# Kernel tuning notes

Hardware: AMD Instinct MI355X
Metric: run time of the kernel (lower is better)

The kernel has to match this reference:

```python
import jax, jax.numpy as jnp
import numpy as np

N = 50000   # nodes
E = 200000  # triplets
IN = 128    # num_in_features
H = 4       # heads
F = 64      # num_out_features
HID = 64    # attention_mlp_hidden


def setup_inputs() -> dict:
    key = jax.random.key(0)
    ks = jax.random.split(key, 12)
    rn = lambda k, shape, s=0.05: (jax.random.normal(k, shape, jnp.float32) * s)
    return {
        "in_nodes_features": jax.random.normal(ks[0], (N, IN), jnp.float32),
        "edge_index": jax.random.randint(ks[1], (3, E), 0, N, jnp.int32),
        "W_proj": rn(ks[2], (H * F, IN)),          # linear_proj (no bias)
        "att_W1": rn(ks[3], (HID, 3 * F)),
        "att_b1": jnp.zeros((HID,), jnp.float32),
        "att_W2": rn(ks[4], (1, HID)),
        "att_b2": jnp.zeros((1,), jnp.float32),
        "e_W1": rn(ks[5], (F, 2 * F)),
        "e_b1": jnp.zeros((F,), jnp.float32),
        "e_W2": rn(ks[6], (F, F)),
        "e_b2": jnp.zeros((F,), jnp.float32),
        "theta": rn(ks[7], (1, H, F), 0.1),
        "bias": jnp.zeros((H * F,), jnp.float32),
    }


def _edge_nn(pair, e_W1, e_b1, e_W2, e_b2):
    # pair: [E, H, 2F] -> [E, H, F]
    h = jax.nn.leaky_relu(jnp.einsum('ehc,fc->ehf', pair, e_W1) + e_b1, 0.2)
    return jnp.einsum('ehf,gf->ehg', h, e_W2) + e_b2


def reference(in_nodes_features, edge_index, W_proj, att_W1, att_b1, att_W2,
              att_b2, e_W1, e_b1, e_W2, e_b2, theta, bias):
    proj = (in_nodes_features @ W_proj.T).reshape(-1, H, F)  # [N, H, F]
    pi = proj[edge_index[0]]  # [E, H, F]
    pj = proj[edge_index[1]]
    pk = proj[edge_index[2]]

    # attention MLP on concatenated triplet features
    comb = jnp.concatenate([pi, pj, pk], axis=-1)            # [E, H, 3F]
    h = jax.nn.relu(jnp.einsum('ehc,dc->ehd', comb, att_W1) + att_b1)
    scores = (jnp.einsum('ehd,od->eho', h, att_W2) + att_b2)[..., 0]  # [E, H]
    scores = jax.nn.leaky_relu(scores, 0.2)
    att = jax.nn.softmax(scores, axis=-1)[..., None]         # softmax over heads, [E, H, 1]

    pairs = [(pj, pk), (pi, pk), (pi, pj)]
    outs = []
    for i in range(3):
        prod = _edge_nn(jnp.concatenate(pairs[i], axis=-1), e_W1, e_b1, e_W2, e_b2)
        ws = jax.ops.segment_sum(att * prod, edge_index[i], num_segments=proj.shape[0])
        outs.append(theta * proj + ws)                       # [N, H, F]

    out = jnp.concatenate(outs, axis=0).reshape(-1, H * F)   # [3N, H*F]
    out = out + bias
    return jax.nn.elu(out)
```

## Files before the change

kernel.cpp:

```cpp
#include <hip/hip_runtime.h>
#include <hip/hip_bf16.h>

#define N_NODES 50000
#define N_EDGES 200000
#define IN_F 128
#define HEADS 4
#define FD 64
#define HF 256
#define NCOLS 1536
#define NT3 (3 * N_NODES)
#define E3  (3 * N_EDGES)
#define TROW 320

#define OFF_PROJ   0UL
#define OFF_TABS   51200000UL
#define OFF_ATT    179200000UL
#define OFF_RANK   182400000UL
#define OFF_ELIST  184800000UL
#define OFF_CNT    187200000UL
#define OFF_OFFS   187800000UL
#define OFF_BSUM   188400008UL
#define OFF_BSW    188401040UL
#define OFF_CB     188794256UL

typedef __attribute__((ext_vector_type(8))) short short8;
typedef __attribute__((ext_vector_type(4))) float f32x4;

__device__ inline short bf16_of(float x) {
    __hip_bfloat16 h = __float2bfloat16(x);
    return *reinterpret_cast<short*>(&h);
}
__device__ inline unsigned pack2(float lo, float hi) {
    return ((unsigned)(unsigned short)bf16_of(hi) << 16) |
           (unsigned)(unsigned short)bf16_of(lo);
}
__device__ inline short8 pack8(float4 a, float4 b) {
    short8 o;
    o[0] = bf16_of(a.x); o[1] = bf16_of(a.y); o[2] = bf16_of(a.z); o[3] = bf16_of(a.w);
    o[4] = bf16_of(b.x); o[5] = bf16_of(b.y); o[6] = bf16_of(b.z); o[7] = bf16_of(b.w);
    return o;
}
__device__ inline void unpk(uint4 v, float* f) {
    f[0] = __uint_as_float(v.x << 16); f[1] = __uint_as_float(v.x & 0xffff0000u);
    f[2] = __uint_as_float(v.y << 16); f[3] = __uint_as_float(v.y & 0xffff0000u);
    f[4] = __uint_as_float(v.z << 16); f[5] = __uint_as_float(v.z & 0xffff0000u);
    f[6] = __uint_as_float(v.w << 16); f[7] = __uint_as_float(v.w & 0xffff0000u);
}
__device__ inline float score8(uint4 ua, uint4 ub, uint4 uc, const float* w) {
    float fa[8], fb[8], fc[8]; unpk(ua, fa); unpk(ub, fb); unpk(uc, fc);
    float p = 0.f;
#pragma unroll
    for (int j = 0; j < 8; ++j) {
        float x = fa[j] + fb[j] + fc[j];
        x = fmaxf(x, 0.f);
        p = fmaf(x, w[j], p);
    }
    return p;
}

__global__ __launch_bounds__(128) void k_comp(const float* __restrict__ Wp,
                                              const float* __restrict__ attW1,
                                              const float* __restrict__ eW1,
                                              const float* __restrict__ attb1,
                                              const float* __restrict__ eb1,
                                              __hip_bfloat16* __restrict__ Bsw,
                                              float* __restrict__ colbias) {
    const int c = blockIdx.x;
    const int k = threadIdx.x;
    float acc;
    float cb = 0.f;
    if (c < HF) {
        acc = Wp[c * IN_F + k];
    } else {
        const int t = (c - HF) >> 8;
        const int rem = (c - HF) & 255;
        const int h = rem >> 6, g = rem & 63;
        const float* T;
        if (t == 0)      T = attW1 + g * 192;
        else if (t == 1) T = attW1 + g * 192 + 64;
        else if (t == 2) T = attW1 + g * 192 + 128;
        else if (t == 3) T = eW1 + g * 128;
        else             T = eW1 + g * 128 + 64;
        acc = 0.f;
        for (int f = 0; f < 64; ++f)
            acc += T[f] * Wp[(h * 64 + f) * IN_F + k];
        if (t == 0) cb = attb1[g];
        else if (t == 3) cb = eb1[g];
    }
    const int ct = c >> 4, cin = c & 15, kin = k & 31, j = k & 7;
    const int ks = k >> 5;
    const int l = cin + ((kin >> 3) << 4);
    Bsw[((ct * 4 + ks) * 64 + l) * 8 + j] = __float2bfloat16(acc);
    if (k == 0) colbias[c] = cb;
}

__global__ __launch_bounds__(256) void k_tab(const float* __restrict__ in,
                                             const __hip_bfloat16* __restrict__ BswH,
                                             const float* __restrict__ colbias,
                                             float* __restrict__ proj,
                                             __hip_bfloat16* __restrict__ tabs) {
    const short8* Bsw = reinterpret_cast<const short8*>(BswH);
    const int lane = threadIdx.x & 63;
    const int wv = threadIdx.x >> 6;
    const int r = lane & 15, q = lane >> 4;
    const int row0 = blockIdx.x * 16;

    short8 a[4];
    const float* ip = in + (size_t)(row0 + r) * IN_F + q * 8;
#pragma unroll
    for (int ks = 0; ks < 4; ++ks)
        a[ks] = pack8(*(const float4*)(ip + ks * 32), *(const float4*)(ip + ks * 32 + 4));

    for (int ctl = 0; ctl < 24; ++ctl) {
        const int ct = wv * 24 + ctl;
        const int c = ct * 16 + r;
        const float cb = colbias[c];
        f32x4 acc = {cb, cb, cb, cb};
#pragma unroll
        for (int ks = 0; ks < 4; ++ks)
            acc = __builtin_amdgcn_mfma_f32_16x16x32_bf16(a[ks], Bsw[(ct * 4 + ks) * 64 + lane], acc, 0, 0, 0);
        if (c < HF) {
#pragma unroll
            for (int i = 0; i < 4; ++i)
                proj[(size_t)(row0 + q * 4 + i) * HF + c] = acc[i];
        } else {
            const int t = (c - HF) >> 8;
            const int rem = (c - HF) & 255;
            const int h = rem >> 6, g = rem & 63;
#pragma unroll
            for (int i = 0; i < 4; ++i)
                tabs[(((size_t)(row0 + q * 4 + i) * HEADS + h) * 5 + t) * 64 + g] =
                    __float2bfloat16(acc[i]);
        }
    }
}

__global__ __launch_bounds__(256) void k_hist(const int* __restrict__ eidx,
                                              int* __restrict__ cnt,
                                              int* __restrict__ rank) {
    const int g = blockIdx.x * 256 + threadIdx.x;
    if (g < E3) {
        const int node = eidx[g];
        const int t = g / N_EDGES;
        rank[g] = atomicAdd(&cnt[t * N_NODES + node], 1);
    }
}

__global__ __launch_bounds__(256) void k_scan1(const int* __restrict__ cnt,
                                               int* __restrict__ offs,
                                               int* __restrict__ bsums) {
    __shared__ int lds[256];
    const int b = blockIdx.x, t = threadIdx.x;
    const int base = b * 1024 + t * 4;
    int v[4];
#pragma unroll
    for (int c = 0; c < 4; ++c) v[c] = (base + c < NT3) ? cnt[base + c] : 0;
    const int s = v[0] + v[1] + v[2] + v[3];
    lds[t] = s;
    __syncthreads();
    for (int off = 1; off < 256; off <<= 1) {
        int x = (t >= off) ? lds[t - off] : 0;
        __syncthreads();
        lds[t] += x;
        __syncthreads();
    }
    if (t == 255) bsums[b] = lds[255];
    int run = lds[t] - s;
#pragma unroll
    for (int c = 0; c < 4; ++c) {
        if (base + c < NT3) offs[base + c] = run;
        run += v[c];
    }
}

__global__ __launch_bounds__(256) void k_scan2(int* __restrict__ bsums, int nb) {
    __shared__ int lds[256];
    const int t = threadIdx.x;
    const int v = (t < nb) ? bsums[t] : 0;
    lds[t] = v;
    __syncthreads();
    for (int off = 1; off < 256; off <<= 1) {
        int x = (t >= off) ? lds[t - off] : 0;
        __syncthreads();
        lds[t] += x;
        __syncthreads();
    }
    if (t < nb) bsums[t] = lds[t] - v;
}

__global__ __launch_bounds__(256) void k_scan3(int* __restrict__ offs,
                                               const int* __restrict__ bsums) {
    const int i = blockIdx.x * 256 + threadIdx.x;
    if (i < NT3) offs[i] += bsums[i >> 10];
    if (i == NT3) offs[NT3] = E3;
}

__global__ __launch_bounds__(256) void k_scat(const int* __restrict__ eidx,
                                              const int* __restrict__ offs,
                                              const int* __restrict__ rank,
                                              int* __restrict__ elist) {
    const int g = blockIdx.x * 256 + threadIdx.x;
    if (g < E3) {
        const int node = eidx[g];
        const int t = g / N_EDGES;
        const int e = g - t * N_EDGES;
        elist[offs[t * N_NODES + node] + rank[g]] = e;
    }
}

__global__ __launch_bounds__(256) void k_att(
        const int* __restrict__ eidx,
        const __hip_bfloat16* __restrict__ tabs,
        const float* __restrict__ attW2, const float* __restrict__ attb2,
        float* __restrict__ attbuf) {
    __shared__ float s_lds[HEADS][16];
    const int lane = threadIdx.x & 63;
    const int h = threadIdx.x >> 6;
    const int r = lane & 15, q = lane >> 4;
    const int e0 = blockIdx.x * 16;

    float awlo[8], awhi[8];
    {
        float4 w0 = *(const float4*)(attW2 + q * 8);
        float4 w1 = *(const float4*)(attW2 + q * 8 + 4);
        awlo[0] = w0.x; awlo[1] = w0.y; awlo[2] = w0.z; awlo[3] = w0.w;
        awlo[4] = w1.x; awlo[5] = w1.y; awlo[6] = w1.z; awlo[7] = w1.w;
        float4 w2 = *(const float4*)(attW2 + 32 + q * 8);
        float4 w3 = *(const float4*)(attW2 + 32 + q * 8 + 4);
        awhi[0] = w2.x; awhi[1] = w2.y; awhi[2] = w2.z; awhi[3] = w2.w;
        awhi[4] = w3.x; awhi[5] = w3.y; awhi[6] = w3.z; awhi[7] = w3.w;
    }
    const float ab2s = attb2[0];

    const int ni = eidx[e0 + r];
    const int nj = eidx[N_EDGES + e0 + r];
    const int nk = eidx[2 * N_EDGES + e0 + r];

    const size_t bi = ((size_t)ni * HEADS + h) * TROW + q * 8;
    const size_t bj = ((size_t)nj * HEADS + h) * TROW + q * 8;
    const size_t bk = ((size_t)nk * HEADS + h) * TROW + q * 8;

    uint4 a0 = *(const uint4*)(tabs + bi);
    uint4 a1 = *(const uint4*)(tabs + bi + 32);
    uint4 b0 = *(const uint4*)(tabs + bj + 64);
    uint4 b1 = *(const uint4*)(tabs + bj + 96);
    uint4 c0 = *(const uint4*)(tabs + bk + 128);
    uint4 c1 = *(const uint4*)(tabs + bk + 160);

    float p = score8(a0, b0, c0, awlo) + score8(a1, b1, c1, awhi);
    p += __shfl_xor(p, 16);
    p += __shfl_xor(p, 32);
    float sc = p + ab2s;
    sc = fmaxf(sc, 0.2f * sc);
    if (lane < 16) s_lds[h][lane] = sc;
    __syncthreads();
    if (lane < 16) {
        const float s0 = s_lds[0][lane], s1 = s_lds[1][lane];
        const float s2 = s_lds[2][lane], s3 = s_lds[3][lane];
        const float mx = fmaxf(fmaxf(s0, s1), fmaxf(s2, s3));
        const float x0 = __expf(s0 - mx), x1 = __expf(s1 - mx);
        const float x2 = __expf(s2 - mx), x3 = __expf(s3 - mx);
        const float rs = 1.f / (x0 + x1 + x2 + x3);
        const float xh = (h == 0) ? x0 : (h == 1) ? x1 : (h == 2) ? x2 : x3;
        attbuf[(size_t)(e0 + lane) * 4 + h] = xh * rs;
    }
}

__global__ __launch_bounds__(256) void k_seg(const int* __restrict__ eidx,
                                             const int* __restrict__ offs,
                                             const int* __restrict__ elist,
                                             const float* __restrict__ attbuf,
                                             const __hip_bfloat16* __restrict__ tabs,
                                             const float* __restrict__ proj,
                                             const float* __restrict__ eW2,
                                             const float* __restrict__ eb2,
                                             const float* __restrict__ theta,
                                             const float* __restrict__ bias,
                                             float* __restrict__ out) {
    __shared__ __hip_bfloat16 S_lds[16][72];
    __shared__ float a_lds[16];
    __shared__ float D_lds[16][68];

    const int lane = threadIdx.x & 63;
    const int w = threadIdx.x >> 6;
    const int h = lane >> 4, r = lane & 15;
    const int q = lane >> 4;
    const int t = blockIdx.y;
    const int n0 = blockIdx.x * 4;
    const int n = n0 + w;
    const int idx = t * N_NODES + n;
    const int p0 = offs[idx], p1 = offs[idx + 1];
    int s0, s1;
    if (t == 0)      { s0 = 1; s1 = 2; }
    else if (t == 1) { s0 = 0; s1 = 2; }
    else             { s0 = 0; s1 = 1; }

    float acc0 = 0.f, acc1 = 0.f, acc2 = 0.f, acc3 = 0.f, alpha = 0.f;
    for (int base = p0; base < p1; base += 4) {
        int ee[4];
#pragma unroll
        for (int c = 0; c < 4; ++c) {
            const int p = base + c;
            ee[c] = elist[p < p1 ? p : p1 - 1];
        }
        int xx[4], yy[4];
        float at[4];
#pragma unroll
        for (int c = 0; c < 4; ++c) {
            xx[c] = eidx[s0 * N_EDGES + ee[c]];
            yy[c] = eidx[s1 * N_EDGES + ee[c]];
        }
#pragma unroll
        for (int c = 0; c < 4; ++c)
            at[c] = (base + c < p1) ? attbuf[(size_t)ee[c] * 4 + h] : 0.f;
        uint2 ua[4], ub[4];
#pragma unroll
        for (int c = 0; c < 4; ++c) {
            ua[c] = *(const uint2*)(tabs + (((size_t)xx[c] * 4 + h) * 5 + 3) * 64 + r * 4);
            ub[c] = *(const uint2*)(tabs + (((size_t)yy[c] * 4 + h) * 5 + 4) * 64 + r * 4);
        }
#pragma unroll
        for (int c = 0; c < 4; ++c) {
            float g0 = __uint_as_float(ua[c].x << 16) + __uint_as_float(ub[c].x << 16);
            float g1 = __uint_as_float(ua[c].x & 0xffff0000u) + __uint_as_float(ub[c].x & 0xffff0000u);
            float g2 = __uint_as_float(ua[c].y << 16) + __uint_as_float(ub[c].y << 16);
            float g3 = __uint_as_float(ua[c].y & 0xffff0000u) + __uint_as_float(ub[c].y & 0xffff0000u);
            g0 = fmaxf(g0, 0.2f * g0); g1 = fmaxf(g1, 0.2f * g1);
            g2 = fmaxf(g2, 0.2f * g2); g3 = fmaxf(g3, 0.2f * g3);
            acc0 = fmaf(at[c], g0, acc0); acc1 = fmaf(at[c], g1, acc1);
            acc2 = fmaf(at[c], g2, acc2); acc3 = fmaf(at[c], g3, acc3);
            alpha += at[c];
        }
    }
    const int tr = w * 4 + h;
    uint2 st;
    st.x = pack2(acc0, acc1);
    st.y = pack2(acc2, acc3);
    *(uint2*)&S_lds[tr][r * 4] = st;
    if (r == 0) a_lds[tr] = alpha;
    __syncthreads();

    {
        const float* wp0 = eW2 + (w * 16 + r) * FD + q * 8;
        const float* wp1 = eW2 + (w * 16 + r) * FD + 32 + q * 8;
        short8 bfr0 = pack8(*(const float4*)wp0, *(const float4*)(wp0 + 4));
        short8 bfr1 = pack8(*(const float4*)wp1, *(const float4*)(wp1 + 4));
        short8 A0 = *(short8*)&S_lds[r][q * 8];
        short8 A1 = *(short8*)&S_lds[r][32 + q * 8];
        f32x4 acc = {0.f, 0.f, 0.f, 0.f};
        acc = __builtin_amdgcn_mfma_f32_16x16x32_bf16(A0, bfr0, acc, 0, 0, 0);
        acc = __builtin_amdgcn_mfma_f32_16x16x32_bf16(A1, bfr1, acc, 0, 0, 0);
#pragma unroll
        for (int i = 0; i < 4; ++i)
            D_lds[q * 4 + i][w * 16 + r] = acc[i];
    }
    __syncthreads();

    const int row = threadIdx.x >> 4;
    const int c4 = threadIdx.x & 15;
    const int f = c4 * 4;
    const int hh = row & 3;
    const int nn = n0 + (row >> 2);
    const size_t rho = ((size_t)t * N_NODES + nn) * 4 + hh;

    float4 Dv = *(float4*)&D_lds[row][f];
    float4 pj = *(const float4*)(proj + (size_t)nn * HF + hh * 64 + f);
    float4 th = *(const float4*)(theta + hh * 64 + f);
    float4 bi = *(const float4*)(bias + hh * 64 + f);
    float4 b2 = *(const float4*)(eb2 + f);
    const float al = a_lds[row];
    float4 o;
    float v;
    v = th.x * pj.x + Dv.x + al * b2.x + bi.x; o.x = v > 0.f ? v : expm1f(v);
    v = th.y * pj.y + Dv.y + al * b2.y + bi.y; o.y = v > 0.f ? v : expm1f(v);
    v = th.z * pj.z + Dv.z + al * b2.z + bi.z; o.z = v > 0.f ? v : expm1f(v);
    v = th.w * pj.w + Dv.w + al * b2.w + bi.w; o.w = v > 0.f ? v : expm1f(v);
    *(float4*)(out + rho * 64 + f) = o;
}

extern "C" void kernel_launch(void* const* d_in, const int* in_sizes, int n_in,
                              void* d_out, int out_size, void* d_ws, size_t ws_size,
                              hipStream_t stream) {
    const float* in_nodes = (const float*)d_in[0];
    const int*   eidx     = (const int*)d_in[1];
    const float* Wp       = (const float*)d_in[2];
    const float* attW1    = (const float*)d_in[3];
    const float* attb1    = (const float*)d_in[4];
    const float* attW2    = (const float*)d_in[5];
    const float* attb2    = (const float*)d_in[6];
    const float* eW1      = (const float*)d_in[7];
    const float* eb1      = (const float*)d_in[8];
    const float* eW2      = (const float*)d_in[9];
    const float* eb2      = (const float*)d_in[10];
    const float* theta    = (const float*)d_in[11];
    const float* bias     = (const float*)d_in[12];

    char* ws = (char*)d_ws;
    float*          proj     = (float*)(ws + OFF_PROJ);
    __hip_bfloat16* tabs     = (__hip_bfloat16*)(ws + OFF_TABS);
    float*          attbuf   = (float*)(ws + OFF_ATT);
    int*            rank     = (int*)(ws + OFF_RANK);
    int*            elist    = (int*)(ws + OFF_ELIST);
    int*            cnt      = (int*)(ws + OFF_CNT);
    int*            offs     = (int*)(ws + OFF_OFFS);
    int*            bsums    = (int*)(ws + OFF_BSUM);
    __hip_bfloat16* Bsw      = (__hip_bfloat16*)(ws + OFF_BSW);
    float*          colbias  = (float*)(ws + OFF_CB);

    float* out = (float*)d_out;

    (void)hipMemsetAsync(cnt, 0, NT3 * sizeof(int), stream);

    k_comp<<<NCOLS, 128, 0, stream>>>(Wp, attW1, eW1, attb1, eb1, Bsw, colbias);
    k_tab<<<N_NODES / 16, 256, 0, stream>>>(in_nodes, Bsw, colbias, proj, tabs);

    k_hist<<<(E3 + 255) / 256, 256, 0, stream>>>(eidx, cnt, rank);
    k_scan1<<<(NT3 + 1023) / 1024, 256, 0, stream>>>(cnt, offs, bsums);
    k_scan2<<<1, 256, 0, stream>>>(bsums, (NT3 + 1023) / 1024);
    k_scan3<<<(NT3 + 256) / 256, 256, 0, stream>>>(offs, bsums);
    k_scat<<<(E3 + 255) / 256, 256, 0, stream>>>(eidx, offs, rank, elist);

    k_att<<<N_EDGES / 16, 256, 0, stream>>>(eidx, tabs, attW2, attb2, attbuf);
    k_seg<<<dim3(N_NODES / 4, 3), 256, 0, stream>>>(eidx, offs, elist, attbuf,
                                                    tabs, proj, eW2, eb2,
                                                    theta, bias, out);
}
```

Baseline: 368.4 us.

## Balance segment-sum edge work across warps within each 4-node block

```diff
diff --git a/kernel.cpp b/kernel.cpp
--- a/kernel.cpp
+++ b/kernel.cpp
@@ -277,6 +277,8 @@
                                              const float* __restrict__ theta,
                                              const float* __restrict__ bias,
                                              float* __restrict__ out) {
+    __shared__ float part[4][16][68];
+    __shared__ float apart[4][16];
     __shared__ __hip_bfloat16 S_lds[16][72];
     __shared__ float a_lds[16];
     __shared__ float D_lds[16][68];
@@ -287,21 +289,31 @@
     const int q = lane >> 4;
     const int t = blockIdx.y;
     const int n0 = blockIdx.x * 4;
-    const int n = n0 + w;
-    const int idx = t * N_NODES + n;
-    const int p0 = offs[idx], p1 = offs[idx + 1];
+    const int idx0 = t * N_NODES + n0;
+    const int o0 = offs[idx0], o1 = offs[idx0 + 1], o2 = offs[idx0 + 2];
+    const int o3 = offs[idx0 + 3], o4 = offs[idx0 + 4];
     int s0, s1;
     if (t == 0)      { s0 = 1; s1 = 2; }
     else if (t == 1) { s0 = 0; s1 = 2; }
     else             { s0 = 0; s1 = 1; }
 
-    float acc0 = 0.f, acc1 = 0.f, acc2 = 0.f, acc3 = 0.f, alpha = 0.f;
-    for (int base = p0; base < p1; base += 4) {
+    const int T = o4 - o0;
+    const int L = (T + 3) >> 2;
+    const int wp0 = o0 + w * L;
+    const int wp1 = min(wp0 + L, o4);
+
+    float c00 = 0.f, c01 = 0.f, c02 = 0.f, c03 = 0.f;
+    float c10 = 0.f, c11 = 0.f, c12 = 0.f, c13 = 0.f;
+    float c20 = 0.f, c21 = 0.f, c22 = 0.f, c23 = 0.f;
+    float c30 = 0.f, c31 = 0.f, c32 = 0.f, c33 = 0.f;
+    float al0 = 0.f, al1 = 0.f, al2 = 0.f, al3 = 0.f;
+
+    for (int bp = wp0; bp < wp1; bp += 4) {
         int ee[4];
 #pragma unroll
         for (int c = 0; c < 4; ++c) {
-            const int p = base + c;
-            ee[c] = elist[p < p1 ? p : p1 - 1];
+            const int p = bp + c;
+            ee[c] = elist[p < wp1 ? p : wp1 - 1];
         }
         int xx[4], yy[4];
         float at[4];
@@ -312,7 +324,7 @@
         }
 #pragma unroll
         for (int c = 0; c < 4; ++c)
-            at[c] = (base + c < p1) ? attbuf[(size_t)ee[c] * 4 + h] : 0.f;
+            at[c] = (bp + c < wp1) ? attbuf[(size_t)ee[c] * 4 + h] : 0.f;
         uint2 ua[4], ub[4];
 #pragma unroll
         for (int c = 0; c < 4; ++c) {
@@ -321,30 +333,70 @@
         }
 #pragma unroll
         for (int c = 0; c < 4; ++c) {
+            const int p = bp + c;
+            const int nl = (p >= o1) + (p >= o2) + (p >= o3);
             float g0 = __uint_as_float(ua[c].x << 16) + __uint_as_float(ub[c].x << 16);
             float g1 = __uint_as_float(ua[c].x & 0xffff0000u) + __uint_as_float(ub[c].x & 0xffff0000u);
             float g2 = __uint_as_float(ua[c].y << 16) + __uint_as_float(ub[c].y << 16);
             float g3 = __uint_as_float(ua[c].y & 0xffff0000u) + __uint_as_float(ub[c].y & 0xffff0000u);
             g0 = fmaxf(g0, 0.2f * g0); g1 = fmaxf(g1, 0.2f * g1);
             g2 = fmaxf(g2, 0.2f * g2); g3 = fmaxf(g3, 0.2f * g3);
-            acc0 = fmaf(at[c], g0, acc0); acc1 = fmaf(at[c], g1, acc1);
-            acc2 = fmaf(at[c], g2, acc2); acc3 = fmaf(at[c], g3, acc3);
-            alpha += at[c];
-        }
-    }
-    const int tr = w * 4 + h;
-    uint2 st;
-    st.x = pack2(acc0, acc1);
-    st.y = pack2(acc2, acc3);
-    *(uint2*)&S_lds[tr][r * 4] = st;
-    if (r == 0) a_lds[tr] = alpha;
-    __syncthreads();
-
+            const float a = at[c];
+            if (nl == 0) {
+                c00 = fmaf(a, g0, c00); c01 = fmaf(a, g1, c01);
+                c02 = fmaf(a, g2, c02); c03 = fmaf(a, g3, c03); al0 += a;
+            } else if (nl == 1) {
+                c10 = fmaf(a, g0, c10); c11 = fmaf(a, g1, c11);
+                c12 = fmaf(a, g2, c12); c13 = fmaf(a, g3, c13); al1 += a;
+            } else if (nl == 2) {
+                c20 = fmaf(a, g0, c20); c21 = fmaf(a, g1, c21);
+                c22 = fmaf(a, g2, c22); c23 = fmaf(a, g3, c23); al2 += a;
+            } else {
+                c30 = fmaf(a, g0, c30); c31 = fmaf(a, g1, c31);
+                c32 = fmaf(a, g2, c32); c33 = fmaf(a, g3, c33); al3 += a;
+            }
+        }
+    }
     {
-        const float* wp0 = eW2 + (w * 16 + r) * FD + q * 8;
-        const float* wp1 = eW2 + (w * 16 + r) * FD + 32 + q * 8;
-        short8 bfr0 = pack8(*(const float4*)wp0, *(const float4*)(wp0 + 4));
-        short8 bfr1 = pack8(*(const float4*)wp1, *(const float4*)(wp1 + 4));
+        f32x4 v0 = {c00, c01, c02, c03};
+        f32x4 v1 = {c10, c11, c12, c13};
+        f32x4 v2 = {c20, c21, c22, c23};
+        f32x4 v3 = {c30, c31, c32, c33};
+        *(f32x4*)&part[w][h][r * 4]      = v0;
+        *(f32x4*)&part[w][4 + h][r * 4]  = v1;
+        *(f32x4*)&part[w][8 + h][r * 4]  = v2;
+        *(f32x4*)&part[w][12 + h][r * 4] = v3;
+        if (r == 0) {
+            apart[w][h] = al0; apart[w][4 + h] = al1;
+            apart[w][8 + h] = al2; apart[w][12 + h] = al3;
+        }
+    }
+    __syncthreads();
+
+    {
+        const int row = threadIdx.x >> 4;
+        const int c4 = (threadIdx.x & 15) * 4;
+        f32x4 s = *(f32x4*)&part[0][row][c4];
+#pragma unroll
+        for (int ww = 1; ww < 4; ++ww) {
+            f32x4 pv = *(f32x4*)&part[ww][row][c4];
+            s.x += pv.x; s.y += pv.y; s.z += pv.z; s.w += pv.w;
+        }
+        uint2 st;
+        st.x = pack2(s.x, s.y);
+        st.y = pack2(s.z, s.w);
+        *(uint2*)&S_lds[row][c4] = st;
+        if (threadIdx.x < 16)
+            a_lds[threadIdx.x] = apart[0][threadIdx.x] + apart[1][threadIdx.x] +
+                                 apart[2][threadIdx.x] + apart[3][threadIdx.x];
+    }
+    __syncthreads();
+
+    {
+        const float* wp0p = eW2 + (w * 16 + r) * FD + q * 8;
+        const float* wp1p = eW2 + (w * 16 + r) * FD + 32 + q * 8;
+        short8 bfr0 = pack8(*(const float4*)wp0p, *(const float4*)(wp0p + 4));
+        short8 bfr1 = pack8(*(const float4*)wp1p, *(const float4*)(wp1p + 4));
         short8 A0 = *(short8*)&S_lds[r][q * 8];
         short8 A1 = *(short8*)&S_lds[r][32 + q * 8];
         f32x4 acc = {0.f, 0.f, 0.f, 0.f};
```

Result: slower. 390.1 us (+5.9%).
